# Optimization experiments

Measured on AMD Instinct MI355X. Metric: run time of the kernel, lower is better.

Reference implementation:

```python
import jax, jax.numpy as jnp
import numpy as np

DIM = 1024
N_HEADS = 16
HEAD_DIM = DIM // N_HEADS
FF_DIM = 4096
EPS = 1e-8


def rms_norm(x, scale):
    # norm = ||x||_2 * d^{-1/2}; out = scale * x / (norm + eps)
    norm = jnp.linalg.norm(x, axis=-1, keepdims=True) * (x.shape[-1] ** -0.5)
    return scale * x / (norm + EPS)


def rope_cos_sin(seq_len, dtype=jnp.float32):
    # inv_freq over even indices of head_dim; after the truncation branch in
    # apply_rotary_pos_emb, effective cos/sin have size head_dim//2.
    inv_freq = 1.0 / (10000.0 ** (jnp.arange(0, HEAD_DIM, 2, dtype=jnp.float32) / HEAD_DIM))
    t = jnp.arange(seq_len, dtype=jnp.float32)
    freqs = t[:, None] * inv_freq[None, :]  # [S, head_dim//2]
    return jnp.cos(freqs).astype(dtype), jnp.sin(freqs).astype(dtype)


def apply_rope(x, cos, sin):
    # x: [B, S, H, hd]; cos/sin: [S, hd//2] broadcast over batch and heads
    c = cos[None, :, None, :]
    s = sin[None, :, None, :]
    x1, x2 = jnp.split(x, 2, axis=-1)
    return jnp.concatenate([x1 * c - x2 * s, x1 * s + x2 * c], axis=-1)


def setup_inputs() -> dict:
    key = jax.random.key(0)
    ks = jax.random.split(key, 10)
    B, S = 2, 2048
    std = DIM ** -0.5
    inp = {
        "x": jax.random.normal(ks[0], (B, S, DIM), jnp.float32),
        "mask": jnp.tril(jnp.ones((S, S), dtype=bool)),
        "qkv_w": jax.random.normal(ks[1], (3 * DIM, DIM), jnp.float32) * std,
        "attn_out_w": jax.random.normal(ks[2], (DIM, DIM), jnp.float32) * std,
        "gate_w": jax.random.normal(ks[3], (FF_DIM, DIM), jnp.float32) * std,
        "gate_b": jnp.zeros((FF_DIM,), jnp.float32),
        "lin_w": jax.random.normal(ks[4], (FF_DIM, DIM), jnp.float32) * std,
        "lin_b": jnp.zeros((FF_DIM,), jnp.float32),
        "ff_out_w": jax.random.normal(ks[5], (DIM, FF_DIM), jnp.float32) * (FF_DIM ** -0.5),
        "norm1_scale": jnp.ones((DIM,), jnp.float32),
        "norm2_scale": jnp.ones((DIM,), jnp.float32),
    }
    return inp


def reference(x, mask, qkv_w, attn_out_w, gate_w, gate_b, lin_w, lin_b,
              ff_out_w, norm1_scale, norm2_scale):
    B, S, _ = x.shape
    residual = x
    qkv = (x @ qkv_w.T).reshape(B, S, 3, N_HEADS, HEAD_DIM)
    q, k, v = qkv[:, :, 0], qkv[:, :, 1], qkv[:, :, 2]  # [B,S,H,hd]
    cos, sin = rope_cos_sin(S, x.dtype)
    q = apply_rope(q, cos, sin)
    k = apply_rope(k, cos, sin)
    # naive full attention, materializing [B,H,S,S] as the source does
    scores = jnp.einsum('bqhd,bkhd->bhqk', q, k) / jnp.sqrt(jnp.asarray(HEAD_DIM, x.dtype))
    scores = jnp.where(mask[None, None, :, :], scores, jnp.asarray(-1e9, x.dtype))
    attn = jax.nn.softmax(scores, axis=-1)
    out = jnp.einsum('bhqk,bkhd->bqhd', attn, v).reshape(B, S, DIM)
    out = out @ attn_out_w.T
    x = rms_norm(residual + out, norm1_scale)
    residual = x
    ff = jax.nn.sigmoid(x @ gate_w.T + gate_b) * (x @ lin_w.T + lin_b)
    ff = ff @ ff_out_w.T
    x = rms_norm(residual + ff, norm2_scale)
    return x
```

## Files before the change

### kernel.cpp

```cpp
#include <hip/hip_runtime.h>
#include <hip/hip_bf16.h>
#include <math.h>

#define DIMSZ 1024
#define NHEAD 16
#define HDIM 64
#define FFDIM 4096
#define SEQ 2048
#define NBATCH 2

typedef unsigned short ushortt;
typedef __attribute__((ext_vector_type(8))) short frag8;
typedef __attribute__((ext_vector_type(4))) float f32x4;

__device__ __forceinline__ float u2f(ushortt u) {
  return __uint_as_float(((unsigned)u) << 16);
}
__device__ __forceinline__ ushortt f2bu(float f) {
  unsigned x = __float_as_uint(f);
  return (ushortt)((x + 0x7FFFu + ((x >> 16) & 1u)) >> 16);
}

__global__ __launch_bounds__(256) void cast_f2b(
    const float* __restrict__ src, ushortt* __restrict__ dst, int n) {
  int i = (blockIdx.x * 256 + threadIdx.x) * 4;
  if (i >= n) return;
  float4 f = *(const float4*)(src + i);
  ushort4 u;
  u.x = f2bu(f.x); u.y = f2bu(f.y); u.z = f2bu(f.z); u.w = f2bu(f.w);
  *(ushort4*)(dst + i) = u;
}

__global__ __launch_bounds__(256) void zero_f32(float* __restrict__ p, int n) {
  int i = (blockIdx.x * 256 + threadIdx.x) * 4;
  if (i < n) *(float4*)(p + i) = make_float4(0.f, 0.f, 0.f, 0.f);
}

template <int EPI, int SK>
__global__ __launch_bounds__(256) void gemm_mfma(
    const ushortt* __restrict__ A, const ushortt* __restrict__ W,
    void* __restrict__ Cv, int M, int N, int K, int KB, size_t skoff) {
  __shared__ __align__(16) short As[2][128 * 32];
  __shared__ __align__(16) short Bs[2][128 * 32];
  const int tid = threadIdx.x;
  const int wave = tid >> 6;
  const int lane = tid & 63;
  int xcd = blockIdx.x & 7, r = blockIdx.x >> 3, kz = 0;
  if (SK == 2) { kz = r & 1; r >>= 1; }
  const int bm = (xcd * 4 + (r & 3)) * 128;
  const int bn = (r >> 2) * 128;
  const int ko0 = kz * KB;
  const int wm = (wave >> 1) * 64;
  const int wn = (wave & 1) * 64;

  f32x4 acc[4][4] = {};

  const int sr = lane >> 2;
  const int sc = (lane & 3) * 8;
  const ushortt* pa0 = A + (size_t)(bm + wave * 16 + sr) * K + ko0 + sc;
  const ushortt* pa1 = pa0 + (size_t)64 * K;
  const ushortt* pb0 = W + (size_t)(bn + wave * 16 + sr) * K + ko0 + sc;
  const ushortt* pb1 = pb0 + (size_t)64 * K;
  const int lo0 = (wave * 16) * 32;
  const int lo1 = (64 + wave * 16) * 32;

  const int fr = lane & 15;
  const int fq = (lane >> 4) * 8;
  const int nt = KB >> 5;

  auto stage = [&](int t, int buf) {
    const int ko = t * 32;
    short* ab = &As[0][0] + buf * 4096;
    short* bb = &Bs[0][0] + buf * 4096;
    __builtin_amdgcn_global_load_lds(
        (const __attribute__((address_space(1))) void*)(pa0 + ko),
        (__attribute__((address_space(3))) void*)(ab + lo0), 16, 0, 0);
    __builtin_amdgcn_global_load_lds(
        (const __attribute__((address_space(1))) void*)(pa1 + ko),
        (__attribute__((address_space(3))) void*)(ab + lo1), 16, 0, 0);
    __builtin_amdgcn_global_load_lds(
        (const __attribute__((address_space(1))) void*)(pb0 + ko),
        (__attribute__((address_space(3))) void*)(bb + lo0), 16, 0, 0);
    __builtin_amdgcn_global_load_lds(
        (const __attribute__((address_space(1))) void*)(pb1 + ko),
        (__attribute__((address_space(3))) void*)(bb + lo1), 16, 0, 0);
  };

  stage(0, 0);

  for (int t = 0; t < nt; ++t) {
    if (t + 1 < nt) {
      stage(t + 1, (t + 1) & 1);
      asm volatile("s_waitcnt vmcnt(4)" ::: "memory");
    } else {
      asm volatile("s_waitcnt vmcnt(0)" ::: "memory");
    }
    __builtin_amdgcn_s_barrier();
    __builtin_amdgcn_sched_barrier(0);
    const short* as = &As[0][0] + (t & 1) * 4096;
    const short* bs = &Bs[0][0] + (t & 1) * 4096;

    frag8 af[4], bf[4];
#pragma unroll
    for (int mi = 0; mi < 4; ++mi)
      af[mi] = *(const frag8*)&as[(wm + mi * 16 + fr) * 32 + fq];
#pragma unroll
    for (int ni = 0; ni < 4; ++ni)
      bf[ni] = *(const frag8*)&bs[(wn + ni * 16 + fr) * 32 + fq];
#pragma unroll
    for (int mi = 0; mi < 4; ++mi)
#pragma unroll
      for (int ni = 0; ni < 4; ++ni)
        acc[mi][ni] = __builtin_amdgcn_mfma_f32_16x16x32_bf16(
            af[mi], bf[ni], acc[mi][ni], 0, 0, 0);
    __builtin_amdgcn_sched_barrier(0);
    __builtin_amdgcn_s_barrier();
  }

  const int er = (lane >> 4) * 4;
  const int ec = lane & 15;
  float* C0 = (float*)Cv + (SK == 2 ? (size_t)kz * skoff : 0);
#pragma unroll
  for (int mi = 0; mi < 4; ++mi)
#pragma unroll
    for (int ni = 0; ni < 4; ++ni)
#pragma unroll
      for (int r2 = 0; r2 < 4; ++r2) {
        int m = bm + wm + mi * 16 + er + r2;
        int n = bn + wn + ni * 16 + ec;
        size_t o = (size_t)m * N + n;
        float v = acc[mi][ni][r2];
        if (EPI == 0) {
          C0[o] = v;
        } else {
          ((ushortt*)Cv)[o] = f2bu(v);
        }
      }
}

__global__ __launch_bounds__(256) void gemm_gatelin(
    const ushortt* __restrict__ A, const ushortt* __restrict__ Wg,
    const ushortt* __restrict__ Wl, ushortt* __restrict__ Cv,
    const float* __restrict__ gbias, const float* __restrict__ lbias,
    int M, int N, int K) {
  __shared__ __align__(16) short As[2][128 * 32];
  __shared__ __align__(16) short Gs[2][128 * 32];
  __shared__ __align__(16) short Ls[2][128 * 32];
  const int tid = threadIdx.x;
  const int wave = tid >> 6;
  const int lane = tid & 63;
  int xcd = blockIdx.x & 7, r = blockIdx.x >> 3;
  const int bm = (xcd * 4 + (r & 3)) * 128;
  const int bn = (r >> 2) * 128;
  const int wm = (wave >> 1) * 64;
  const int wn = (wave & 1) * 64;

  f32x4 accg[4][4] = {};
  f32x4 accl[4][4] = {};

  const int sr = lane >> 2;
  const int sc = (lane & 3) * 8;
  const ushortt* pa0 = A + (size_t)(bm + wave * 16 + sr) * K + sc;
  const ushortt* pa1 = pa0 + (size_t)64 * K;
  const ushortt* pg0 = Wg + (size_t)(bn + wave * 16 + sr) * K + sc;
  const ushortt* pg1 = pg0 + (size_t)64 * K;
  const ushortt* pl0 = Wl + (size_t)(bn + wave * 16 + sr) * K + sc;
  const ushortt* pl1 = pl0 + (size_t)64 * K;
  const int lo0 = (wave * 16) * 32;
  const int lo1 = (64 + wave * 16) * 32;

  const int fr = lane & 15;
  const int fq = (lane >> 4) * 8;
  const int nt = K >> 5;

  auto stage = [&](int t, int buf) {
    const int ko = t * 32;
    short* ab = &As[0][0] + buf * 4096;
    short* gb = &Gs[0][0] + buf * 4096;
    short* lb = &Ls[0][0] + buf * 4096;
    __builtin_amdgcn_global_load_lds(
        (const __attribute__((address_space(1))) void*)(pa0 + ko),
        (__attribute__((address_space(3))) void*)(ab + lo0), 16, 0, 0);
    __builtin_amdgcn_global_load_lds(
        (const __attribute__((address_space(1))) void*)(pa1 + ko),
        (__attribute__((address_space(3))) void*)(ab + lo1), 16, 0, 0);
    __builtin_amdgcn_global_load_lds(
        (const __attribute__((address_space(1))) void*)(pg0 + ko),
        (__attribute__((address_space(3))) void*)(gb + lo0), 16, 0, 0);
    __builtin_amdgcn_global_load_lds(
        (const __attribute__((address_space(1))) void*)(pg1 + ko),
        (__attribute__((address_space(3))) void*)(gb + lo1), 16, 0, 0);
    __builtin_amdgcn_global_load_lds(
        (const __attribute__((address_space(1))) void*)(pl0 + ko),
        (__attribute__((address_space(3))) void*)(lb + lo0), 16, 0, 0);
    __builtin_amdgcn_global_load_lds(
        (const __attribute__((address_space(1))) void*)(pl1 + ko),
        (__attribute__((address_space(3))) void*)(lb + lo1), 16, 0, 0);
  };

  stage(0, 0);

  for (int t = 0; t < nt; ++t) {
    if (t + 1 < nt) {
      stage(t + 1, (t + 1) & 1);
      asm volatile("s_waitcnt vmcnt(6)" ::: "memory");
    } else {
      asm volatile("s_waitcnt vmcnt(0)" ::: "memory");
    }
    __builtin_amdgcn_s_barrier();
    __builtin_amdgcn_sched_barrier(0);
    const short* as = &As[0][0] + (t & 1) * 4096;
    const short* gs = &Gs[0][0] + (t & 1) * 4096;
    const short* ls = &Ls[0][0] + (t & 1) * 4096;

    frag8 af[4], gf[4], lf[4];
#pragma unroll
    for (int mi = 0; mi < 4; ++mi)
      af[mi] = *(const frag8*)&as[(wm + mi * 16 + fr) * 32 + fq];
#pragma unroll
    for (int ni = 0; ni < 4; ++ni) {
      gf[ni] = *(const frag8*)&gs[(wn + ni * 16 + fr) * 32 + fq];
      lf[ni] = *(const frag8*)&ls[(wn + ni * 16 + fr) * 32 + fq];
    }
#pragma unroll
    for (int mi = 0; mi < 4; ++mi)
#pragma unroll
      for (int ni = 0; ni < 4; ++ni) {
        accg[mi][ni] = __builtin_amdgcn_mfma_f32_16x16x32_bf16(
            af[mi], gf[ni], accg[mi][ni], 0, 0, 0);
        accl[mi][ni] = __builtin_amdgcn_mfma_f32_16x16x32_bf16(
            af[mi], lf[ni], accl[mi][ni], 0, 0, 0);
      }
    __builtin_amdgcn_sched_barrier(0);
    __builtin_amdgcn_s_barrier();
  }

  const int er = (lane >> 4) * 4;
  const int ec = lane & 15;
#pragma unroll
  for (int mi = 0; mi < 4; ++mi)
#pragma unroll
    for (int ni = 0; ni < 4; ++ni)
#pragma unroll
      for (int r2 = 0; r2 < 4; ++r2) {
        int m = bm + wm + mi * 16 + er + r2;
        int n = bn + wn + ni * 16 + ec;
        size_t o = (size_t)m * N + n;
        float g = accg[mi][ni][r2] + gbias[n];
        float l = accl[mi][ni][r2] + lbias[n];
        float sig = 1.0f / (1.0f + __expf(-g));
        ((ushortt*)Cv)[o] = f2bu(sig * l);
      }
}

__global__ __launch_bounds__(256) void gemm_ffout(
    const ushortt* __restrict__ A, const float* __restrict__ Bw,
    float* __restrict__ C, int koff) {
  __shared__ __align__(16) short As[2][128 * 32];
  __shared__ __align__(16) short Bs[2][128 * 32];
  const int tid = threadIdx.x;
  const int wave = tid >> 6;
  const int lane = tid & 63;
  int xcd = blockIdx.x & 7, r = blockIdx.x >> 3;
  const int kz = r & 1; r >>= 1;
  const int bm = (xcd * 4 + (r & 3)) * 128;
  const int bn = (r >> 2) * 128;
  const int wm = (wave >> 1) * 64;
  const int wn = (wave & 1) * 64;

  f32x4 acc[4][4] = {};

  const int sr = lane >> 2;
  const int sc = (lane & 3) * 8;
  const ushortt* pa0 = A + (size_t)(bm + wave * 16 + sr) * 2048 + kz * 1024 + sc;
  const ushortt* pa1 = pa0 + (size_t)64 * 2048;
  const int lo0 = (wave * 16) * 32;
  const int lo1 = (64 + wave * 16) * 32;

  const int br = tid >> 2;
  const int kc = (tid & 3) * 8;
  const float* pb0 = Bw + (size_t)(bn + br) * FFDIM + koff + kz * 1024 + kc;
  const float* pb1 = pb0 + (size_t)64 * FFDIM;

  const int fr = lane & 15;
  const int fq = (lane >> 4) * 8;
  const int nt = 1024 >> 5;

  float4 f0, f1, f2, f3;
  auto bload = [&](int t) {
    const float* p0 = pb0 + t * 32;
    const float* p1 = pb1 + t * 32;
    f0 = *(const float4*)p0; f1 = *(const float4*)(p0 + 4);
    f2 = *(const float4*)p1; f3 = *(const float4*)(p1 + 4);
  };
  auto pk = [&](float4 a, float4 b) {
    frag8 v;
    v[0] = (short)f2bu(a.x); v[1] = (short)f2bu(a.y);
    v[2] = (short)f2bu(a.z); v[3] = (short)f2bu(a.w);
    v[4] = (short)f2bu(b.x); v[5] = (short)f2bu(b.y);
    v[6] = (short)f2bu(b.z); v[7] = (short)f2bu(b.w);
    return v;
  };
  auto bwrite = [&](int buf) {
    *(frag8*)&Bs[buf][tid * 8] = pk(f0, f1);
    *(frag8*)&Bs[buf][2048 + tid * 8] = pk(f2, f3);
  };
  auto astage = [&](int t, int buf) {
    const int ko = t * 32;
    short* ab = &As[0][0] + buf * 4096;
    __builtin_amdgcn_global_load_lds(
        (const __attribute__((address_space(1))) void*)(pa0 + ko),
        (__attribute__((address_space(3))) void*)(ab + lo0), 16, 0, 0);
    __builtin_amdgcn_global_load_lds(
        (const __attribute__((address_space(1))) void*)(pa1 + ko),
        (__attribute__((address_space(3))) void*)(ab + lo1), 16, 0, 0);
  };

  bload(0);
  astage(0, 0);
  bwrite(0);
  asm volatile("s_waitcnt lgkmcnt(0)" ::: "memory");

  for (int t = 0; t < nt; ++t) {
    if (t + 1 < nt) {
      bload(t + 1);
      astage(t + 1, (t + 1) & 1);
      asm volatile("s_waitcnt vmcnt(6)" ::: "memory");
    } else {
      asm volatile("s_waitcnt vmcnt(0)" ::: "memory");
    }
    __builtin_amdgcn_s_barrier();
    __builtin_amdgcn_sched_barrier(0);
    const short* as = &As[0][0] + (t & 1) * 4096;
    const short* bs = &Bs[0][0] + (t & 1) * 4096;

    frag8 af[4], bf[4];
#pragma unroll
    for (int mi = 0; mi < 4; ++mi)
      af[mi] = *(const frag8*)&as[(wm + mi * 16 + fr) * 32 + fq];
#pragma unroll
    for (int ni = 0; ni < 4; ++ni)
      bf[ni] = *(const frag8*)&bs[(wn + ni * 16 + fr) * 32 + fq];
#pragma unroll
    for (int mi = 0; mi < 4; ++mi)
#pragma unroll
      for (int ni = 0; ni < 4; ++ni)
        acc[mi][ni] = __builtin_amdgcn_mfma_f32_16x16x32_bf16(
            af[mi], bf[ni], acc[mi][ni], 0, 0, 0);
    if (t + 1 < nt) bwrite((t + 1) & 1);
    asm volatile("s_waitcnt lgkmcnt(0)" ::: "memory");
    __builtin_amdgcn_sched_barrier(0);
    __builtin_amdgcn_s_barrier();
  }

  const int er = (lane >> 4) * 4;
  const int ec = lane & 15;
#pragma unroll
  for (int mi = 0; mi < 4; ++mi)
#pragma unroll
    for (int ni = 0; ni < 4; ++ni)
#pragma unroll
      for (int r2 = 0; r2 < 4; ++r2) {
        int m = bm + wm + mi * 16 + er + r2;
        int n = bn + wn + ni * 16 + ec;
        unsafeAtomicAdd(C + (size_t)m * 1024 + n, acc[mi][ni][r2]);
      }
}

__global__ __launch_bounds__(256) void rope_prep(
    const ushortt* __restrict__ qkv, ushortt* __restrict__ Qr,
    ushortt* __restrict__ Kr, ushortt* __restrict__ Vr) {
  const int s0 = blockIdx.x * 64;
  const int bh = blockIdx.y;
  const int b = bh >> 4, h = bh & 15;
  const int tid = threadIdx.x;
  __shared__ float ifr_s[32];
  __shared__ ushortt vt[64][72];
  if (tid < 32) ifr_s[tid] = __powf(10000.0f, -(float)tid * (1.0f / 32.0f));
  __syncthreads();
  const size_t qbase = (size_t)bh * SEQ * 64;

#pragma unroll
  for (int i = 0; i < 8; ++i) {
    int p = i * 256 + tid;
    int r = p >> 5, d = p & 31;
    size_t src = ((size_t)(b * SEQ + s0 + r)) * (3 * DIMSZ) + h * 64 + d;
    float q1 = u2f(qkv[src]), q2 = u2f(qkv[src + 32]);
    float k1 = u2f(qkv[src + DIMSZ]), k2 = u2f(qkv[src + DIMSZ + 32]);
    float ang = (float)(s0 + r) * ifr_s[d];
    float sn, cs;
    __sincosf(ang, &sn, &cs);
    size_t dst = qbase + (size_t)(s0 + r) * 64 + d;
    Qr[dst]      = f2bu((q1 * cs - q2 * sn) * 0.125f);
    Qr[dst + 32] = f2bu((q1 * sn + q2 * cs) * 0.125f);
    Kr[dst]      = f2bu(k1 * cs - k2 * sn);
    Kr[dst + 32] = f2bu(k1 * sn + k2 * cs);
  }

#pragma unroll
  for (int i = 0; i < 2; ++i) {
    int e = (i * 256 + tid) * 8;
    int r = e >> 6, d0 = e & 63;
    size_t src = ((size_t)(b * SEQ + s0 + r)) * (3 * DIMSZ) + 2 * DIMSZ + h * 64 + d0;
    *(ushort4*)&vt[r][d0]     = *(const ushort4*)(qkv + src);
    *(ushort4*)&vt[r][d0 + 4] = *(const ushort4*)(qkv + src + 4);
  }
  __syncthreads();
  {
    int d = tid >> 2;
    int sc0 = (tid & 3) * 16;
    size_t dst = (size_t)bh * 64 * SEQ + (size_t)blockIdx.x * 4096 +
                 (size_t)d * 64 + sc0;
    ushortt tmp[16];
#pragma unroll
    for (int j = 0; j < 16; ++j) tmp[j] = vt[sc0 + j][d];
    *(ushort4*)(Vr + dst)      = *(ushort4*)&tmp[0];
    *(ushort4*)(Vr + dst + 4)  = *(ushort4*)&tmp[4];
    *(ushort4*)(Vr + dst + 8)  = *(ushort4*)&tmp[8];
    *(ushort4*)(Vr + dst + 12) = *(ushort4*)&tmp[12];
  }
}

__global__ __launch_bounds__(512) void flash_mfma(
    const ushortt* __restrict__ Qr, const ushortt* __restrict__ Kr,
    const ushortt* __restrict__ Vr, ushortt* __restrict__ ctx) {
  const int id = blockIdx.x;
  const int r5 = id & 255;
  const int qt0 = r5 >> 5;
  const int qt = (id & 256) ? (15 - qt0) : qt0;
  const int bh = r5 & 31;
  const int q0 = qt * 128;
  const int b = bh >> 4, h = bh & 15;
  const int tid = threadIdx.x;
  const int w = tid >> 6;
  const int lane = tid & 63;
  const int fr = lane & 15;
  const int quad = lane >> 4;

  __shared__ __align__(16) short Kb[2][4096];
  __shared__ __align__(16) short Vb[2][4096];
  __shared__ __align__(16) ushortt Ps[8][16][72];

  const size_t qkbase = (size_t)bh * SEQ * 64;
  const size_t vbase = (size_t)bh * 64 * SEQ;

  const int lin = (w << 10) + ((lane & 63) << 4);
  const int swz = lin ^ (((lin >> 7) & 7) << 4);
  const char* ksrc = (const char*)(Kr + qkbase) + swz;
  const char* vsrc = (const char*)(Vr + vbase) + swz;
  short* kdst[2] = {&Kb[0][w * 512], &Kb[1][w * 512]};
  short* vdst[2] = {&Vb[0][w * 512], &Vb[1][w * 512]};

  frag8 aq[2];
#pragma unroll
  for (int hh = 0; hh < 2; ++hh)
    aq[hh] = *(const frag8*)(Qr + qkbase + (size_t)(q0 + w * 16 + fr) * 64 +
                             hh * 32 + quad * 8);

  float mr[4], lr[4];
  f32x4 od[4] = {};
#pragma unroll
  for (int r = 0; r < 4; ++r) { mr[r] = -1e30f; lr[r] = 0.0f; }

  const int nt = 2 * qt + 2;

  __builtin_amdgcn_global_load_lds(
      (const __attribute__((address_space(1))) void*)ksrc,
      (__attribute__((address_space(3))) void*)kdst[0], 16, 0, 0);
  __builtin_amdgcn_global_load_lds(
      (const __attribute__((address_space(1))) void*)vsrc,
      (__attribute__((address_space(3))) void*)vdst[0], 16, 0, 0);

  for (int t = 0; t < nt; ++t) {
    const int c0 = t * 64;
    if (t + 1 < nt) {
      const char* kn = ksrc + (size_t)(t + 1) * 8192;
      const char* vn = vsrc + (size_t)(t + 1) * 8192;
      __builtin_amdgcn_global_load_lds(
          (const __attribute__((address_space(1))) void*)kn,
          (__attribute__((address_space(3))) void*)kdst[(t + 1) & 1], 16, 0, 0);
      __builtin_amdgcn_global_load_lds(
          (const __attribute__((address_space(1))) void*)vn,
          (__attribute__((address_space(3))) void*)vdst[(t + 1) & 1], 16, 0, 0);
      asm volatile("s_waitcnt vmcnt(2)" ::: "memory");
    } else {
      asm volatile("s_waitcnt vmcnt(0)" ::: "memory");
    }
    __builtin_amdgcn_s_barrier();
    __builtin_amdgcn_sched_barrier(0);
    const char* kcur = (const char*)Kb[t & 1];
    const char* vcur = (const char*)Vb[t & 1];

    if (c0 <= q0 + w * 16 + 15) {
      f32x4 sc[4] = {};
#pragma unroll
      for (int ni = 0; ni < 4; ++ni)
#pragma unroll
        for (int hh = 0; hh < 2; ++hh) {
          int kb = (((ni * 16 + fr) << 7) + (hh << 6) + (quad << 4)) ^
                   ((fr & 7) << 4);
          frag8 kf = *(const frag8*)(kcur + kb);
          sc[ni] = __builtin_amdgcn_mfma_f32_16x16x32_bf16(aq[hh], kf, sc[ni],
                                                           0, 0, 0);
        }

      if (c0 + 63 > q0 + w * 16) {
        int rowb = q0 + w * 16 + quad * 4;
#pragma unroll
        for (int ni = 0; ni < 4; ++ni) {
          int col = c0 + ni * 16 + fr;
#pragma unroll
          for (int r = 0; r < 4; ++r)
            if (col > rowb + r) sc[ni][r] = -1e30f;
        }
      }

#pragma unroll
      for (int r = 0; r < 4; ++r) {
        float cm = fmaxf(fmaxf(sc[0][r], sc[1][r]), fmaxf(sc[2][r], sc[3][r]));
        for (int off = 1; off < 16; off <<= 1)
          cm = fmaxf(cm, __shfl_xor(cm, off, 16));
        float mn = fmaxf(mr[r], cm);
        float corr = __expf(mr[r] - mn);
        mr[r] = mn;
        float ps = 0.0f;
#pragma unroll
        for (int ni = 0; ni < 4; ++ni) {
          float p = __expf(sc[ni][r] - mn);
          Ps[w][quad * 4 + r][ni * 16 + fr] = f2bu(p);
          ps += p;
        }
        for (int off = 1; off < 16; off <<= 1) ps += __shfl_xor(ps, off, 16);
        lr[r] = lr[r] * corr + ps;
#pragma unroll
        for (int dt = 0; dt < 4; ++dt) od[dt][r] *= corr;
      }

      frag8 pf[2];
#pragma unroll
      for (int hh = 0; hh < 2; ++hh)
        pf[hh] = *(const frag8*)&Ps[w][fr][hh * 32 + quad * 8];
#pragma unroll
      for (int dt = 0; dt < 4; ++dt)
#pragma unroll
        for (int hh = 0; hh < 2; ++hh) {
          int vb_ = (((dt * 16 + fr) << 7) + (hh << 6) + (quad << 4)) ^
                    ((fr & 7) << 4);
          frag8 vf = *(const frag8*)(vcur + vb_);
          od[dt] = __builtin_amdgcn_mfma_f32_16x16x32_bf16(pf[hh], vf, od[dt],
                                                           0, 0, 0);
        }
    }
    __builtin_amdgcn_sched_barrier(0);
    __builtin_amdgcn_s_barrier();
  }

#pragma unroll
  for (int r = 0; r < 4; ++r) {
    float inv = 1.0f / lr[r];
    size_t row = (size_t)(b * SEQ + q0 + w * 16 + quad * 4 + r) * DIMSZ + h * 64;
#pragma unroll
    for (int dt = 0; dt < 4; ++dt)
      ctx[row + dt * 16 + fr] = f2bu(od[dt][r] * inv);
  }
}

template <int DUAL, int NP>
__global__ __launch_bounds__(256) void add_rmsnorm(
    const float* __restrict__ res, const float* __restrict__ pa,
    const float* __restrict__ pb, const float* __restrict__ scale,
    float* __restrict__ out, ushortt* __restrict__ out2) {
  const int row = blockIdx.x;
  const int tid = threadIdx.x;
  const size_t base = (size_t)row * DIMSZ;
  __shared__ float red[4];
  float y[4];
  float ss = 0.0f;
#pragma unroll
  for (int j = 0; j < 4; ++j) {
    int d = tid + j * 256;
    float yv = res[base + d] + pa[base + d];
    if (NP == 3) yv += pb[base + d];
    y[j] = yv;
    ss += yv * yv;
  }
  for (int off = 1; off < 64; off <<= 1) ss += __shfl_xor(ss, off, 64);
  if ((tid & 63) == 0) red[tid >> 6] = ss;
  __syncthreads();
  float tot = red[0] + red[1] + red[2] + red[3];
  float norm = sqrtf(tot) * 0.03125f;
  float inv = 1.0f / (norm + 1e-8f);
#pragma unroll
  for (int j = 0; j < 4; ++j) {
    int d = tid + j * 256;
    float v = scale[d] * y[j] * inv;
    out[base + d] = v;
    if (DUAL) out2[base + d] = f2bu(v);
  }
}

extern "C" void kernel_launch(void* const* d_in, const int* in_sizes, int n_in,
                              void* d_out, int out_size, void* d_ws, size_t ws_size,
                              hipStream_t stream) {
  const float* x          = (const float*)d_in[0];
  const float* qkv_w      = (const float*)d_in[2];
  const float* attn_out_w = (const float*)d_in[3];
  const float* gate_w     = (const float*)d_in[4];
  const float* gate_b     = (const float*)d_in[5];
  const float* lin_w      = (const float*)d_in[6];
  const float* lin_b      = (const float*)d_in[7];
  const float* ff_out_w   = (const float*)d_in[8];
  const float* n1s        = (const float*)d_in[9];
  const float* n2s        = (const float*)d_in[10];
  float* out = (float*)d_out;

  const int M = NBATCH * SEQ;
  char* ws = (char*)d_ws;
  char* dob = (char*)d_out;
  const size_t MB = 1 << 20;
  ushortt* qkv_tmp = (ushortt*)(ws + 0);
  ushortt* xb      = (ushortt*)(ws + 24 * MB);
  ushortt* qkv_wb  = (ushortt*)(ws + 32 * MB);
  ushortt* Qr      = (ushortt*)(ws + 24 * MB);
  ushortt* Kr      = (ushortt*)(ws + 32 * MB);
  ushortt* Vr      = (ushortt*)(ws + 40 * MB);
  ushortt* attn_wb = (ushortt*)(ws + 24 * MB);
  float*   proj_a  = (float*)(ws + 0);
  float*   proj_b  = (float*)(ws + 40 * MB);
  float*   x1      = (float*)(ws + 16 * MB);
  ushortt* x1b     = (ushortt*)(ws + 32 * MB);
  float*   proj2   = (float*)(ws + 0);
  ushortt* gcb     = (ushortt*)(ws + 40 * MB);
  ushortt* lcb     = (ushortt*)(ws + 44 * MB);
  ushortt* ctx  = (ushortt*)(dob + 0);
  ushortt* ffc  = (ushortt*)(dob + 0);

  cast_f2b<<<4194304 / 1024, 256, 0, stream>>>(x, xb, 4194304);
  cast_f2b<<<3145728 / 1024, 256, 0, stream>>>(qkv_w, qkv_wb, 3145728);
  gemm_mfma<1, 1><<<(3072 / 128) * 32, 256, 0, stream>>>(
      xb, qkv_wb, qkv_tmp, M, 3072, DIMSZ, DIMSZ, 0);
  rope_prep<<<dim3(SEQ / 64, NBATCH * NHEAD), 256, 0, stream>>>(
      qkv_tmp, Qr, Kr, Vr);
  flash_mfma<<<(SEQ / 128) * NBATCH * NHEAD, 512, 0, stream>>>(
      Qr, Kr, Vr, ctx);
  cast_f2b<<<1048576 / 1024, 256, 0, stream>>>(attn_out_w, attn_wb, 1048576);
  gemm_mfma<0, 2><<<(DIMSZ / 128) * 32 * 2, 256, 0, stream>>>(
      ctx, attn_wb, proj_a, M, DIMSZ, DIMSZ, 512,
      (size_t)(40 * MB) / sizeof(float));
  add_rmsnorm<1, 3><<<M, 256, 0, stream>>>(x, proj_a, proj_b, n1s, x1, x1b);
  zero_f32<<<4194304 / 1024, 256, 0, stream>>>(proj2, 4194304);
  for (int c = 0; c < 2; ++c) {
    cast_f2b<<<2048, 256, 0, stream>>>(
        gate_w + (size_t)c * 2097152, gcb, 2097152);
    cast_f2b<<<2048, 256, 0, stream>>>(
        lin_w + (size_t)c * 2097152, lcb, 2097152);
    gemm_gatelin<<<(2048 / 128) * 32, 256, 0, stream>>>(
        x1b, gcb, lcb, ffc, gate_b + c * 2048, lin_b + c * 2048,
        M, 2048, DIMSZ);
    gemm_ffout<<<(1024 / 128) * 32 * 2, 256, 0, stream>>>(
        ffc, ff_out_w, proj2, c * 2048);
  }
  add_rmsnorm<0, 2><<<M, 256, 0, stream>>>(x1, proj2, nullptr, n2s, out,
                                           nullptr);
}
```

Baseline: 558.0 us.

## Prefetch gatelin weights via registers, fuse weight casts and accumulator zeroing

The gate/lin GEMM now loads weight tiles into registers two K-steps ahead and writes them to LDS after the MFMAs, while the activation tile uses a triple-buffered direct-to-LDS load. This is meant to hide global latency better. The two per-chunk weight casts are merged into one launch, and the ff-out accumulator is zeroed inside the first add+RMSNorm through its aliased buffer rather than by a separate kernel. The more complex waitcnt bookkeeping risks subtle ordering errors and adds register pressure.

```diff
diff --git a/kernel.cpp b/kernel.cpp
--- a/kernel.cpp
+++ b/kernel.cpp
@@ -31,9 +31,21 @@
   *(ushort4*)(dst + i) = u;
 }
 
-__global__ __launch_bounds__(256) void zero_f32(float* __restrict__ p, int n) {
+__global__ __launch_bounds__(256) void cast_gl(
+    const float* __restrict__ g, const float* __restrict__ l,
+    ushortt* __restrict__ gd, ushortt* __restrict__ ld, int n) {
   int i = (blockIdx.x * 256 + threadIdx.x) * 4;
-  if (i < n) *(float4*)(p + i) = make_float4(0.f, 0.f, 0.f, 0.f);
+  const float* src;
+  ushortt* dst;
+  if (i < n) {
+    src = g + i; dst = gd + i;
+  } else {
+    int j = i - n; src = l + j; dst = ld + j;
+  }
+  float4 f = *(const float4*)src;
+  ushort4 u;
+  u.x = f2bu(f.x); u.y = f2bu(f.y); u.z = f2bu(f.z); u.w = f2bu(f.w);
+  *(ushort4*)dst = u;
 }
 
 template <int EPI, int SK>
@@ -143,7 +155,7 @@
     const ushortt* __restrict__ Wl, ushortt* __restrict__ Cv,
     const float* __restrict__ gbias, const float* __restrict__ lbias,
     int M, int N, int K) {
-  __shared__ __align__(16) short As[2][128 * 32];
+  __shared__ __align__(16) short As[3][128 * 32];
   __shared__ __align__(16) short Gs[2][128 * 32];
   __shared__ __align__(16) short Ls[2][128 * 32];
   const int tid = threadIdx.x;
@@ -162,54 +174,69 @@
   const int sc = (lane & 3) * 8;
   const ushortt* pa0 = A + (size_t)(bm + wave * 16 + sr) * K + sc;
   const ushortt* pa1 = pa0 + (size_t)64 * K;
-  const ushortt* pg0 = Wg + (size_t)(bn + wave * 16 + sr) * K + sc;
-  const ushortt* pg1 = pg0 + (size_t)64 * K;
-  const ushortt* pl0 = Wl + (size_t)(bn + wave * 16 + sr) * K + sc;
-  const ushortt* pl1 = pl0 + (size_t)64 * K;
   const int lo0 = (wave * 16) * 32;
   const int lo1 = (64 + wave * 16) * 32;
+
+  const int br = tid >> 2;
+  const int kc = (tid & 3) * 8;
+  const ushortt* pg = Wg + (size_t)(bn + br) * K + kc;
+  const ushortt* pl = Wl + (size_t)(bn + br) * K + kc;
 
   const int fr = lane & 15;
   const int fq = (lane >> 4) * 8;
   const int nt = K >> 5;
 
-  auto stage = [&](int t, int buf) {
+  auto astage = [&](int t, int buf) {
     const int ko = t * 32;
     short* ab = &As[0][0] + buf * 4096;
-    short* gb = &Gs[0][0] + buf * 4096;
-    short* lb = &Ls[0][0] + buf * 4096;
     __builtin_amdgcn_global_load_lds(
         (const __attribute__((address_space(1))) void*)(pa0 + ko),
         (__attribute__((address_space(3))) void*)(ab + lo0), 16, 0, 0);
     __builtin_amdgcn_global_load_lds(
         (const __attribute__((address_space(1))) void*)(pa1 + ko),
         (__attribute__((address_space(3))) void*)(ab + lo1), 16, 0, 0);
-    __builtin_amdgcn_global_load_lds(
-        (const __attribute__((address_space(1))) void*)(pg0 + ko),
-        (__attribute__((address_space(3))) void*)(gb + lo0), 16, 0, 0);
-    __builtin_amdgcn_global_load_lds(
-        (const __attribute__((address_space(1))) void*)(pg1 + ko),
-        (__attribute__((address_space(3))) void*)(gb + lo1), 16, 0, 0);
-    __builtin_amdgcn_global_load_lds(
-        (const __attribute__((address_space(1))) void*)(pl0 + ko),
-        (__attribute__((address_space(3))) void*)(lb + lo0), 16, 0, 0);
-    __builtin_amdgcn_global_load_lds(
-        (const __attribute__((address_space(1))) void*)(pl1 + ko),
-        (__attribute__((address_space(3))) void*)(lb + lo1), 16, 0, 0);
   };
 
-  stage(0, 0);
-
-  for (int t = 0; t < nt; ++t) {
-    if (t + 1 < nt) {
-      stage(t + 1, (t + 1) & 1);
+  frag8 gA0, gA1, lA0, lA1;
+  frag8 gB0, gB1, lB0, lB1;
+
+  gA0 = *(const frag8*)(pg);
+  gA1 = *(const frag8*)(pg + (size_t)64 * K);
+  lA0 = *(const frag8*)(pl);
+  lA1 = *(const frag8*)(pl + (size_t)64 * K);
+  astage(0, 0);
+  gB0 = *(const frag8*)(pg + 32);
+  gB1 = *(const frag8*)(pg + (size_t)64 * K + 32);
+  lB0 = *(const frag8*)(pl + 32);
+  lB1 = *(const frag8*)(pl + (size_t)64 * K + 32);
+  astage(1, 1);
+  *(frag8*)&Gs[0][tid * 8] = gA0;
+  *(frag8*)&Gs[0][2048 + tid * 8] = gA1;
+  *(frag8*)&Ls[0][tid * 8] = lA0;
+  *(frag8*)&Ls[0][2048 + tid * 8] = lA1;
+  asm volatile("s_waitcnt lgkmcnt(0)" ::: "memory");
+  __builtin_amdgcn_s_barrier();
+
+  int a0 = 0, a1 = 1, a2 = 2;
+
+  auto body = [&](int t, frag8& ldg0, frag8& ldg1, frag8& ldl0, frag8& ldl1,
+                  frag8& wrg0, frag8& wrg1, frag8& wrl0, frag8& wrl1) {
+    if (t + 2 < nt) {
+      const int ko = (t + 2) * 32;
+      ldg0 = *(const frag8*)(pg + ko);
+      ldg1 = *(const frag8*)(pg + (size_t)64 * K + ko);
+      ldl0 = *(const frag8*)(pl + ko);
+      ldl1 = *(const frag8*)(pl + (size_t)64 * K + ko);
+      astage(t + 2, a2);
+      asm volatile("s_waitcnt vmcnt(12)" ::: "memory");
+    } else if (t + 1 < nt) {
       asm volatile("s_waitcnt vmcnt(6)" ::: "memory");
     } else {
       asm volatile("s_waitcnt vmcnt(0)" ::: "memory");
     }
     __builtin_amdgcn_s_barrier();
     __builtin_amdgcn_sched_barrier(0);
-    const short* as = &As[0][0] + (t & 1) * 4096;
+    const short* as = &As[0][0] + a0 * 4096;
     const short* gs = &Gs[0][0] + (t & 1) * 4096;
     const short* ls = &Ls[0][0] + (t & 1) * 4096;
 
@@ -231,8 +258,23 @@
         accl[mi][ni] = __builtin_amdgcn_mfma_f32_16x16x32_bf16(
             af[mi], lf[ni], accl[mi][ni], 0, 0, 0);
       }
+    if (t + 1 < nt) {
+      short* gd = &Gs[0][0] + ((t + 1) & 1) * 4096;
+      short* ld = &Ls[0][0] + ((t + 1) & 1) * 4096;
+      *(frag8*)&gd[tid * 8] = wrg0;
+      *(frag8*)&gd[2048 + tid * 8] = wrg1;
+      *(frag8*)&ld[tid * 8] = wrl0;
+      *(frag8*)&ld[2048 + tid * 8] = wrl1;
+    }
+    asm volatile("s_waitcnt lgkmcnt(0)" ::: "memory");
     __builtin_amdgcn_sched_barrier(0);
     __builtin_amdgcn_s_barrier();
+    int tmp = a0; a0 = a1; a1 = a2; a2 = tmp;
+  };
+
+  for (int t = 0; t < nt; t += 2) {
+    body(t, gA0, gA1, lA0, lA1, gB0, gB1, lB0, lB1);
+    body(t + 1, gB0, gB1, lB0, lB1, gA0, gA1, lA0, lA1);
   }
 
   const int er = (lane >> 4) * 4;
@@ -565,9 +607,9 @@
   }
 }
 
-template <int DUAL, int NP>
+template <int DUAL, int NP, int ZR>
 __global__ __launch_bounds__(256) void add_rmsnorm(
-    const float* __restrict__ res, const float* __restrict__ pa,
+    const float* __restrict__ res, float* __restrict__ pa,
     const float* __restrict__ pb, const float* __restrict__ scale,
     float* __restrict__ out, ushortt* __restrict__ out2) {
   const int row = blockIdx.x;
@@ -582,6 +624,7 @@
     float yv = res[base + d] + pa[base + d];
     if (NP == 3) yv += pb[base + d];
     y[j] = yv;
+    if (ZR) pa[base + d] = 0.0f;
     ss += yv * yv;
   }
   for (int off = 1; off < 64; off <<= 1) ss += __shfl_xor(ss, off, 64);
@@ -647,19 +690,17 @@
   gemm_mfma<0, 2><<<(DIMSZ / 128) * 32 * 2, 256, 0, stream>>>(
       ctx, attn_wb, proj_a, M, DIMSZ, DIMSZ, 512,
       (size_t)(40 * MB) / sizeof(float));
-  add_rmsnorm<1, 3><<<M, 256, 0, stream>>>(x, proj_a, proj_b, n1s, x1, x1b);
-  zero_f32<<<4194304 / 1024, 256, 0, stream>>>(proj2, 4194304);
+  add_rmsnorm<1, 3, 1><<<M, 256, 0, stream>>>(x, proj_a, proj_b, n1s, x1, x1b);
   for (int c = 0; c < 2; ++c) {
-    cast_f2b<<<2048, 256, 0, stream>>>(
-        gate_w + (size_t)c * 2097152, gcb, 2097152);
-    cast_f2b<<<2048, 256, 0, stream>>>(
-        lin_w + (size_t)c * 2097152, lcb, 2097152);
+    cast_gl<<<4096, 256, 0, stream>>>(
+        gate_w + (size_t)c * 2097152, lin_w + (size_t)c * 2097152,
+        gcb, lcb, 2097152);
     gemm_gatelin<<<(2048 / 128) * 32, 256, 0, stream>>>(
         x1b, gcb, lcb, ffc, gate_b + c * 2048, lin_b + c * 2048,
         M, 2048, DIMSZ);
     gemm_ffout<<<(1024 / 128) * 32 * 2, 256, 0, stream>>>(
         ffc, ff_out_w, proj2, c * 2048);
   }
-  add_rmsnorm<0, 2><<<M, 256, 0, stream>>>(x1, proj2, nullptr, n2s, out,
-                                           nullptr);
-}
+  add_rmsnorm<0, 2, 0><<<M, 256, 0, stream>>>(x1, proj2, nullptr, n2s, out,
+                                              nullptr);
+}
```

After: 572.3 us. +2.6%, slower.
